# Optimization experiments

Hardware: AMD Instinct MI355X
Metric: run time of the kernel (lower is better)

The kernel has to match this reference:

```python
import jax, jax.numpy as jnp
import numpy as np

B, NF, N, D, S, H = 16, 16, 1024, 128, 8, 128
EPS = 1e-8
SCALE = D ** -0.5


def _ln(x, g, b):
    m = x.mean(-1, keepdims=True)
    v = ((x - m) ** 2).mean(-1, keepdims=True)
    return (x - m) / jnp.sqrt(v + 1e-5) * g + b


def setup_inputs() -> dict:
    key = jax.random.key(0)
    ks = jax.random.split(key, 16)
    w = lambda k, *s: jax.random.normal(k, s, jnp.float32) * 0.02
    return {
        'inputs': jax.random.normal(ks[0], (B, NF, N, D), jnp.float32),
        'slots_init': jax.random.normal(ks[1], (1, S, D), jnp.float32),
        'Wq': w(ks[2], D, D), 'bq': jnp.zeros((D,), jnp.float32),
        'Wk': w(ks[3], D, D), 'bk': jnp.zeros((D,), jnp.float32),
        'Wv': w(ks[4], D, D), 'bv': jnp.zeros((D,), jnp.float32),
        'W1': w(ks[5], H, D), 'b1': jnp.zeros((H,), jnp.float32),
        'W2': w(ks[6], D, H), 'b2': jnp.zeros((D,), jnp.float32),
        'Wih': w(ks[7], 3 * D, D), 'Whh': w(ks[8], 3 * D, D),
        'bih': jnp.zeros((3 * D,), jnp.float32), 'bhh': jnp.zeros((3 * D,), jnp.float32),
        'g_in': jnp.ones((D,), jnp.float32), 'be_in': jnp.zeros((D,), jnp.float32),
        'g_sl': jnp.ones((D,), jnp.float32), 'be_sl': jnp.zeros((D,), jnp.float32),
        'g_ff': jnp.ones((D,), jnp.float32), 'be_ff': jnp.zeros((D,), jnp.float32),
    }


def reference(inputs, slots_init, Wq, bq, Wk, bk, Wv, bv, W1, b1, W2, b2,
              Wih, Whh, bih, bhh, g_in, be_in, g_sl, be_sl, g_ff, be_ff):
    def gru(x, h):  # PyTorch GRUCell, x/h: [BS, D]
        gi = x @ Wih.T + bih
        gh = h @ Whh.T + bhh
        r = jax.nn.sigmoid(gi[:, :D] + gh[:, :D])
        z = jax.nn.sigmoid(gi[:, D:2 * D] + gh[:, D:2 * D])
        n = jnp.tanh(gi[:, 2 * D:] + r * gh[:, 2 * D:])
        return (1.0 - z) * n + z * h

    def get_attention(slots, x):  # slots [B,S,D], x [B,N,D]
        slots_prev = slots
        xn = _ln(x, g_in, be_in)
        k = xn @ Wk.T + bk
        v = xn @ Wv.T + bv
        q = _ln(slots, g_sl, be_sl) @ Wq.T + bq
        dots = jnp.einsum('bid,bjd->bij', q, k) * SCALE  # [B,S,N]
        attn_ori = jax.nn.softmax(dots, axis=1) + EPS    # softmax over slots
        attn = attn_ori / attn_ori.sum(axis=-1, keepdims=True)
        updates = jnp.einsum('bjd,bij->bid', v, attn)    # [B,S,D]
        slots = gru(updates.reshape(-1, D), slots_prev.reshape(-1, D)).reshape(slots.shape[0], -1, D)
        ff = jax.nn.relu(_ln(slots, g_ff, be_ff) @ W1.T + b1) @ W2.T + b2
        return slots + ff, attn_ori

    slots = jnp.broadcast_to(slots_init, (inputs.shape[0], S, D))
    slots, _ = get_attention(slots, inputs[:, 0])  # warm-up on frame 0

    def body(carry, x_f):
        s, a = get_attention(carry, x_f)
        return s, (s, a)

    _, (slots_seq, attn_seq) = jax.lax.scan(body, slots, jnp.moveaxis(inputs, 1, 0))
    slots_out = jnp.moveaxis(slots_seq, 0, 1)  # [B,NF,S,D]
    attns = jnp.moveaxis(attn_seq, 0, 1)       # [B,NF,S,N]
    return slots_out, attns
```

## Files before the change

kernel.cpp:

```cpp
#include <hip/hip_runtime.h>

#define B_ 16
#define NF_ 16
#define N_ 1024
#define D_ 128
#define S_ 8
#define SCALE_ 0.08838834764831845f
#define NB 256
#define NT 512

struct SmemA {
  float Xt[64 * 129];
  float qWs[1024];
  float at[512];
  float rowsum[64], rowsum2[64];
  float qbs[8];
};
struct SmemB {
  float Pk[128], upd[128], hn[128], buf[128], hid[128], qsh[128], nrm[128];
  float gi[384], gh[384];
  float red[4], ssm;
};
union Smem { SmemA a; SmemB b; };

__device__ __forceinline__ float gload(const float* p) {
  return __hip_atomic_load(p, __ATOMIC_RELAXED, __HIP_MEMORY_SCOPE_AGENT);
}
__device__ __forceinline__ void gstore(float* p, float v) {
  __hip_atomic_store(p, v, __ATOMIC_RELAXED, __HIP_MEMORY_SCOPE_AGENT);
}

__device__ __forceinline__ void arrive(unsigned* c) {
  __syncthreads();
  if (threadIdx.x == 0) {
    __builtin_amdgcn_s_waitcnt(0);
    __hip_atomic_fetch_add(c, 1u, __ATOMIC_RELAXED, __HIP_MEMORY_SCOPE_AGENT);
  }
}
__device__ __forceinline__ void wait_for(unsigned* c, unsigned target) {
  if (threadIdx.x == 0) {
    while (__hip_atomic_load(c, __ATOMIC_RELAXED, __HIP_MEMORY_SCOPE_AGENT) < target)
      __builtin_amdgcn_s_sleep(1);
  }
  __syncthreads();
}

__device__ __forceinline__ float dot128f(const float* __restrict__ wrow, const float* x, float acc) {
  const float4* w = (const float4*)wrow;
#pragma unroll
  for (int i = 0; i < 32; ++i) {
    float4 v = w[i];
    const float4 xv = *(const float4*)(x + i * 4);
    acc += v.x * xv.x + v.y * xv.y + v.z * xv.z + v.w * xv.w;
  }
  return acc;
}

__device__ __forceinline__ void stats128(float v, int t, float* red, float& m, float& inv, float eps) {
  __syncthreads();
  float s = (t < 128) ? v : 0.f;
  float s2 = (t < 128) ? v * v : 0.f;
#pragma unroll
  for (int off = 32; off; off >>= 1) { s += __shfl_down(s, off); s2 += __shfl_down(s2, off); }
  if (t == 0)  { red[0] = s; red[2] = s2; }
  if (t == 64) { red[1] = s; red[3] = s2; }
  __syncthreads();
  m = (red[0] + red[1]) * (1.f / 128.f);
  float var = (red[2] + red[3]) * (1.f / 128.f) - m * m;
  inv = rsqrtf(var + eps);
}

__device__ __forceinline__ float sigm(float x) { return 1.f / (1.f + __expf(-x)); }
__device__ __forceinline__ float tanh_f(float x) { return 1.f - 2.f / (1.f + __expf(2.f * x)); }

__device__ void q_project(SmemB& B, const float* slot,
    const float* __restrict__ g_sl, const float* __restrict__ be_sl,
    const float* __restrict__ Wq, const float* __restrict__ bq,
    const float* __restrict__ Wk, const float* __restrict__ bk,
    float* qW_g, float* qb_g, int bs) {
  int t = threadIdx.x;
  float m, inv;
  float sv = (t < 128) ? slot[t] : 0.f;
  stats128(sv, t, B.red, m, inv, 1e-5f);
  if (t < 128) B.nrm[t] = (sv - m) * inv * g_sl[t] + be_sl[t];
  __syncthreads();
  if (t < 128) B.qsh[t] = dot128f(Wq + t * 128, B.nrm, bq[t]);
  __syncthreads();
  if (t < 128) {
    float a = 0.f;
#pragma unroll 16
    for (int d = 0; d < 128; ++d) a += B.qsh[d] * Wk[d * 128 + t];
    gstore(&qW_g[bs * 128 + t], a);
    float p = B.qsh[t] * bk[t];
#pragma unroll
    for (int off = 32; off; off >>= 1) p += __shfl_down(p, off);
    if (t == 0)  B.red[0] = p;
    if (t == 64) B.red[1] = p;
  }
  __syncthreads();
  if (t == 0) gstore(&qb_g[bs], B.red[0] + B.red[1]);
}

__global__ __launch_bounds__(NT) void slot_persist(
    const float* __restrict__ x, const float* __restrict__ slots_init,
    const float* __restrict__ Wq, const float* __restrict__ bq,
    const float* __restrict__ Wk, const float* __restrict__ bk,
    const float* __restrict__ Wv, const float* __restrict__ bv,
    const float* __restrict__ W1, const float* __restrict__ b1,
    const float* __restrict__ W2, const float* __restrict__ b2,
    const float* __restrict__ Wih, const float* __restrict__ Whh,
    const float* __restrict__ bih, const float* __restrict__ bhh,
    const float* __restrict__ g_in, const float* __restrict__ be_in,
    const float* __restrict__ g_sl, const float* __restrict__ be_sl,
    const float* __restrict__ g_ff, const float* __restrict__ be_ff,
    float* out_slots, float* out_attn,
    unsigned* cntA, unsigned* cntB,
    float* qW_g, float* qb_g, float* P_part, float* S_part) {
  __shared__ __align__(16) Smem sm;
  __shared__ __align__(16) float slot_sh[128];
  __shared__ float gs[128], bs_[128];
  int t = threadIdx.x, bid = blockIdx.x;
  int b = bid >> 4, jt = bid & 15;
  bool isB = (jt < 8);
  unsigned* cA = cntA + (b << 6);
  unsigned* cB = cntB + (b << 6);

  if (t < 128) { gs[t] = g_in[t]; bs_[t] = be_in[t]; }
  if (isB) {
    if (t < 128) slot_sh[t] = slots_init[jt * 128 + t];
    q_project(sm.b, slot_sh, g_sl, be_sl, Wq, bq, Wk, bk, qW_g, qb_g, b * 8 + jt);
    arrive(cB);
  }
  float4 pf[4];
  {
    const float* xsrc = x + (((long)b * NF_ + 0) * N_ + jt * 64) * D_;
#pragma unroll
    for (int i = 0; i < 4; ++i) {
      int ch = t + i * 512;
      pf[i] = *(const float4*)(xsrc + (ch >> 5) * 128 + (ch & 31) * 4);
    }
  }
  wait_for(cB, 8u);

  for (int it = 0; it < 17; ++it) {
    int f = (it == 0) ? 0 : it - 1;
    int wo = it > 0;
#pragma unroll
    for (int i = 0; i < 4; ++i) {
      int ch = t + i * 512;
      float* dst = sm.a.Xt + (ch >> 5) * 129 + (ch & 31) * 4;
      dst[0] = pf[i].x; dst[1] = pf[i].y; dst[2] = pf[i].z; dst[3] = pf[i].w;
    }
    sm.a.qWs[t] = gload(&qW_g[b * 1024 + t]);
    sm.a.qWs[512 + t] = gload(&qW_g[b * 1024 + 512 + t]);
    if (t < 8) sm.a.qbs[t] = gload(&qb_g[b * 8 + t]);
    __syncthreads();
    int r8 = t >> 3, p8 = t & 7;
    {
      const float* row = sm.a.Xt + r8 * 129 + p8 * 16;
      float s1 = 0.f, s2 = 0.f;
#pragma unroll
      for (int i = 0; i < 16; ++i) { float v = row[i]; s1 += v; s2 += v * v; }
      s1 += __shfl_down(s1, 1); s2 += __shfl_down(s2, 1);
      s1 += __shfl_down(s1, 2); s2 += __shfl_down(s2, 2);
      s1 += __shfl_down(s1, 4); s2 += __shfl_down(s2, 4);
      if (p8 == 0) { sm.a.rowsum[r8] = s1; sm.a.rowsum2[r8] = s2; }
    }
    __syncthreads();
    {
      float m = sm.a.rowsum[r8] * (1.f / 128.f);
      float var = sm.a.rowsum2[r8] * (1.f / 128.f) - m * m;
      float inv = rsqrtf(var + 1e-5f);
      float* row = sm.a.Xt + r8 * 129 + p8 * 16;
      const float* gg = gs + p8 * 16;
      const float* bb = bs_ + p8 * 16;
#pragma unroll
      for (int i = 0; i < 16; ++i) row[i] = (row[i] - m) * inv * gg[i] + bb[i];
    }
    __syncthreads();
    {
      int s = t >> 6, j = t & 63;
      const float* qq = sm.a.qWs + s * 128;
      const float* xr = sm.a.Xt + j * 129;
      float d = 0.f;
#pragma unroll
      for (int k = 0; k < 128; ++k) d += xr[k] * qq[k];
      sm.a.at[s * 64 + j] = (d + sm.a.qbs[s]) * SCALE_;
    }
    __syncthreads();
    if (t < 64) {
      float vals[8], mx = -1e30f;
#pragma unroll
      for (int s = 0; s < 8; ++s) { vals[s] = sm.a.at[s * 64 + t]; mx = fmaxf(mx, vals[s]); }
      float sum = 0.f;
#pragma unroll
      for (int s = 0; s < 8; ++s) { vals[s] = __expf(vals[s] - mx); sum += vals[s]; }
      float rr = 1.f / sum;
#pragma unroll
      for (int s = 0; s < 8; ++s) { vals[s] = vals[s] * rr + 1e-8f; sm.a.at[s * 64 + t] = vals[s]; }
      if (wo) {
#pragma unroll
        for (int s = 0; s < 8; ++s)
          out_attn[(((long)b * NF_ + f) * S_ + s) * N_ + jt * 64 + t] = vals[s];
      }
    }
    __syncthreads();
    {
      int w = t >> 6, lane = t & 63;
      float v = sm.a.at[w * 64 + lane];
#pragma unroll
      for (int off = 32; off; off >>= 1) v += __shfl_down(v, off);
      if (lane == 0) gstore(&S_part[(b * 16 + jt) * 8 + w], v);
    }
    {
      int k2 = t & 127, h = t >> 7;
      float u0 = 0.f, u1 = 0.f;
      const float* a0 = sm.a.at + h * 64;
      const float* a1 = sm.a.at + (h + 4) * 64;
#pragma unroll 8
      for (int j = 0; j < 64; ++j) {
        float xv = sm.a.Xt[j * 129 + k2];
        u0 += xv * a0[j]; u1 += xv * a1[j];
      }
      float* pp = P_part + (long)(b * 16 + jt) * 8 * 128;
      gstore(&pp[h * 128 + k2], u0);
      gstore(&pp[(h + 4) * 128 + k2], u1);
    }
    arrive(cA);
    if (it < 16) {
      const float* xsrc = x + (((long)b * NF_ + it) * N_ + jt * 64) * D_;
#pragma unroll
      for (int i = 0; i < 4; ++i) {
        int ch = t + i * 512;
        pf[i] = *(const float4*)(xsrc + (ch >> 5) * 128 + (ch & 31) * 4);
      }
    }
    if (isB) {
      wait_for(cA, 16u * (it + 1));
      SmemB& B = sm.b;
      int s = jt;
      if (t < 128) {
        float pa = 0.f;
#pragma unroll
        for (int j = 0; j < 16; ++j)
          pa += gload(&P_part[(long)((b * 16 + j) * 8 + s) * 128 + t]);
        B.Pk[t] = pa;
      }
      if (t < 16) {
        float sv = gload(&S_part[(b * 16 + t) * 8 + s]);
        sv += __shfl_down(sv, 8); sv += __shfl_down(sv, 4);
        sv += __shfl_down(sv, 2); sv += __shfl_down(sv, 1);
        if (t == 0) B.ssm = sv;
      }
      __syncthreads();
      if (t < 128) {
        float a = dot128f(Wv + t * 128, B.Pk, 0.f);
        B.upd[t] = a / B.ssm + bv[t];
      } else {
        int r = t - 128;
        B.gh[r] = dot128f(Whh + r * 128, slot_sh, bhh[r]);
      }
      __syncthreads();
      if (t < 384) B.gi[t] = dot128f(Wih + t * 128, B.upd, bih[t]);
      __syncthreads();
      if (t < 128) {
        float r = sigm(B.gi[t] + B.gh[t]);
        float z = sigm(B.gi[128 + t] + B.gh[128 + t]);
        float n = tanh_f(B.gi[256 + t] + r * B.gh[256 + t]);
        B.hn[t] = (1.f - z) * n + z * slot_sh[t];
      }
      float m, inv;
      float hv = (t < 128) ? B.hn[t] : 0.f;
      stats128(hv, t, B.red, m, inv, 1e-5f);
      if (t < 128) B.buf[t] = (hv - m) * inv * g_ff[t] + be_ff[t];
      __syncthreads();
      if (t < 128) B.hid[t] = fmaxf(dot128f(W1 + t * 128, B.buf, b1[t]), 0.f);
      __syncthreads();
      if (t < 128) {
        float ffv = dot128f(W2 + t * 128, B.hid, b2[t]);
        float sn = B.hn[t] + ffv;
        slot_sh[t] = sn;
        if (wo) out_slots[(((long)b * NF_ + f) * S_ + s) * D_ + t] = sn;
      }
      __syncthreads();
      if (it < 16) {
        q_project(B, slot_sh, g_sl, be_sl, Wq, bq, Wk, bk, qW_g, qb_g, b * 8 + s);
        arrive(cB);
        wait_for(cB, 8u * (it + 2));
      }
    } else {
      if (it < 16) wait_for(cB, 8u * (it + 2));
    }
  }
}

extern "C" void kernel_launch(void* const* d_in, const int* in_sizes, int n_in,
                              void* d_out, int out_size, void* d_ws, size_t ws_size,
                              hipStream_t stream) {
  const float* inputs     = (const float*)d_in[0];
  const float* slots_init = (const float*)d_in[1];
  const float* Wq  = (const float*)d_in[2];
  const float* bq  = (const float*)d_in[3];
  const float* Wk  = (const float*)d_in[4];
  const float* bk  = (const float*)d_in[5];
  const float* Wv  = (const float*)d_in[6];
  const float* bv  = (const float*)d_in[7];
  const float* W1  = (const float*)d_in[8];
  const float* b1  = (const float*)d_in[9];
  const float* W2  = (const float*)d_in[10];
  const float* b2  = (const float*)d_in[11];
  const float* Wih = (const float*)d_in[12];
  const float* Whh = (const float*)d_in[13];
  const float* bih = (const float*)d_in[14];
  const float* bhh = (const float*)d_in[15];
  const float* g_in  = (const float*)d_in[16];
  const float* be_in = (const float*)d_in[17];
  const float* g_sl  = (const float*)d_in[18];
  const float* be_sl = (const float*)d_in[19];
  const float* g_ff  = (const float*)d_in[20];
  const float* be_ff = (const float*)d_in[21];

  float* out_slots = (float*)d_out;
  float* out_attn  = out_slots + (size_t)B_ * NF_ * S_ * D_;

  char* ws = (char*)d_ws;
  unsigned* cntA = (unsigned*)ws;
  unsigned* cntB = (unsigned*)(ws + 4096);
  float* qW_g    = (float*)(ws + 16384);
  float* qb_g    = (float*)(ws + 16384 + 65536);
  float* P_part  = (float*)(ws + 16384 + 66048);
  float* S_part  = (float*)(ws + 16384 + 66048 + 1048576);

  hipMemsetAsync(d_ws, 0, 16384, stream);

  slot_persist<<<NB, NT, 0, stream>>>(inputs, slots_init, Wq, bq, Wk, bk, Wv, bv,
      W1, b1, W2, b2, Wih, Whh, bih, bhh, g_in, be_in, g_sl, be_sl, g_ff, be_ff,
      out_slots, out_attn, cntA, cntB, qW_g, qb_g, P_part, S_part);
}
```

Before: 775.8 us.

## Fold LayerNorm and projections into precomputed weights, one grid barrier per frame

A precompute kernel now builds fused weight products once: Wih·Wv, the Wk-Wq product, and the matching bias terms. The input LayerNorm is folded algebraically into the attention logits and the update, so keys and values are never materialized. The persistent kernel is restructured to 128 blocks of 1024 threads, each handling 128 tokens and all 8 slots. Every block redundantly recomputes the GRU, the MLP and the next query, which removes the second cross-block barrier and the separate slot-update blocks. Partial sums are double-buffered by parity. The cost is duplicated slot work in each block and heavier shared-memory staging of weights.

```diff
diff --git a/kernel.cpp b/kernel.cpp
--- a/kernel.cpp
+++ b/kernel.cpp
@@ -5,23 +5,33 @@
 #define N_ 1024
 #define D_ 128
 #define S_ 8
+#define NT 1024
 #define SCALE_ 0.08838834764831845f
-#define NB 256
-#define NT 512
-
-struct SmemA {
-  float Xt[64 * 129];
-  float qWs[1024];
-  float at[512];
-  float rowsum[64], rowsum2[64];
-  float qbs[8];
+
+struct PA {
+  float X[128 * 129];
+  float at[8 * 132];
+  float ap[8 * 132];
+  float mean[128], rinv[128];
 };
-struct SmemB {
-  float Pk[128], upd[128], hn[128], buf[128], hid[128], qsh[128], nrm[128];
-  float gi[384], gh[384];
-  float red[4], ssm;
+struct PB {
+  float WL[128 * 132];
+  float part[4 * 8 * 128];
+  float Pn[8 * 132];
+  float gh[8 * 388];
+  float gi[8 * 388];
+  float hn[8 * 132];
+  float buf[8 * 132];
+  float hid[8 * 132];
 };
-union Smem { SmemA a; SmemB b; };
+union SMU { PA a; PB b; };
+struct Per {
+  float h[8 * 132];
+  float gqW[8 * 132];
+  float gI[128], bI[128], gF[128], bF[128], gS[128], bS[128];
+  float c0s[8], c1s[8], qbs[8], ssp[8], mbp[8], invSS[8];
+  float red[48];
+};
 
 __device__ __forceinline__ float gload(const float* p) {
   return __hip_atomic_load(p, __ATOMIC_RELAXED, __HIP_MEMORY_SCOPE_AGENT);
@@ -29,7 +39,6 @@
 __device__ __forceinline__ void gstore(float* p, float v) {
   __hip_atomic_store(p, v, __ATOMIC_RELAXED, __HIP_MEMORY_SCOPE_AGENT);
 }
-
 __device__ __forceinline__ void arrive(unsigned* c) {
   __syncthreads();
   if (threadIdx.x == 0) {
@@ -44,253 +53,360 @@
   }
   __syncthreads();
 }
-
-__device__ __forceinline__ float dot128f(const float* __restrict__ wrow, const float* x, float acc) {
-  const float4* w = (const float4*)wrow;
-#pragma unroll
-  for (int i = 0; i < 32; ++i) {
-    float4 v = w[i];
-    const float4 xv = *(const float4*)(x + i * 4);
-    acc += v.x * xv.x + v.y * xv.y + v.z * xv.z + v.w * xv.w;
-  }
-  return acc;
-}
-
-__device__ __forceinline__ void stats128(float v, int t, float* red, float& m, float& inv, float eps) {
-  __syncthreads();
-  float s = (t < 128) ? v : 0.f;
-  float s2 = (t < 128) ? v * v : 0.f;
-#pragma unroll
-  for (int off = 32; off; off >>= 1) { s += __shfl_down(s, off); s2 += __shfl_down(s2, off); }
-  if (t == 0)  { red[0] = s; red[2] = s2; }
-  if (t == 64) { red[1] = s; red[3] = s2; }
-  __syncthreads();
-  m = (red[0] + red[1]) * (1.f / 128.f);
-  float var = (red[2] + red[3]) * (1.f / 128.f) - m * m;
-  inv = rsqrtf(var + eps);
-}
-
 __device__ __forceinline__ float sigm(float x) { return 1.f / (1.f + __expf(-x)); }
 __device__ __forceinline__ float tanh_f(float x) { return 1.f - 2.f / (1.f + __expf(2.f * x)); }
 
-__device__ void q_project(SmemB& B, const float* slot,
-    const float* __restrict__ g_sl, const float* __restrict__ be_sl,
+__device__ __forceinline__ void stage_w(float* WL, const float* __restrict__ W, int t) {
+#pragma unroll
+  for (int i = 0; i < 4; ++i) {
+    int idx = t + i * 1024;
+    int r = idx >> 5, k4 = idx & 31;
+    const float4 v = *(const float4*)(W + r * 128 + k4 * 4);
+    *(float4*)&WL[r * 132 + ((k4 ^ (r & 7)) << 2)] = v;
+  }
+}
+
+__device__ __forceinline__ void wmat8(SMU& sm, const float* vecs, int t) {
+  if (t < 512) {
+    int r = t & 127, kc = t >> 7;
+    float acc[8] = {0.f,0.f,0.f,0.f,0.f,0.f,0.f,0.f};
+#pragma unroll
+    for (int g = 0; g < 8; ++g) {
+      int k4 = kc * 8 + g;
+      const float4 wv = *(const float4*)&sm.b.WL[r * 132 + ((k4 ^ (r & 7)) << 2)];
+#pragma unroll
+      for (int s2 = 0; s2 < 8; ++s2) {
+        const float4 vv = *(const float4*)&vecs[s2 * 132 + k4 * 4];
+        acc[s2] += wv.x * vv.x + wv.y * vv.y + wv.z * vv.z + wv.w * vv.w;
+      }
+    }
+#pragma unroll
+    for (int s2 = 0; s2 < 8; ++s2) sm.b.part[(kc * 8 + s2) * 128 + r] = acc[s2];
+  }
+}
+
+__device__ void slot_to_qw(SMU& sm, Per& P,
+    const float* __restrict__ Wqk, const float* __restrict__ bqk,
+    const float* __restrict__ wqbk, const float* __restrict__ bqbk, int t) {
+  int s = t >> 7, d = t & 127, w = t >> 6, lane = t & 63;
+  float v = P.h[s * 132 + d];
+  float a1 = v, a2 = v * v;
+#pragma unroll
+  for (int off = 32; off; off >>= 1) { a1 += __shfl_down(a1, off); a2 += __shfl_down(a2, off); }
+  if (lane == 0) { P.red[w] = a1; P.red[16 + w] = a2; }
+  __syncthreads();
+  float m = (P.red[2 * s] + P.red[2 * s + 1]) * (1.f / 128.f);
+  float var = (P.red[16 + 2 * s] + P.red[16 + 2 * s + 1]) * (1.f / 128.f) - m * m;
+  float inv = rsqrtf(var + 1e-5f);
+  float nv = (v - m) * inv * P.gS[d] + P.bS[d];
+  sm.b.buf[s * 132 + d] = nv;
+  float qp = wqbk[d] * nv;
+#pragma unroll
+  for (int off = 32; off; off >>= 1) qp += __shfl_down(qp, off);
+  if (lane == 0) P.red[32 + w] = qp;
+  stage_w(sm.b.WL, Wqk, t);
+  __syncthreads();
+  if (t < 8) P.qbs[t] = P.red[32 + 2 * t] + P.red[32 + 2 * t + 1] + bqbk[0];
+  wmat8(sm, sm.b.buf, t);
+  __syncthreads();
+  {
+    int r = d;
+    float qv = bqk[r];
+#pragma unroll
+    for (int kc = 0; kc < 4; ++kc) qv += sm.b.part[(kc * 8 + s) * 128 + r];
+    float gq = P.gI[r] * qv;
+    P.gqW[s * 132 + r] = gq;
+    float p1 = gq, p0 = P.bI[r] * qv;
+#pragma unroll
+    for (int off = 32; off; off >>= 1) { p1 += __shfl_down(p1, off); p0 += __shfl_down(p0, off); }
+    if (lane == 0) { P.red[w] = p1; P.red[16 + w] = p0; }
+  }
+  __syncthreads();
+  if (t < 8) {
+    P.c1s[t] = P.red[2 * t] + P.red[2 * t + 1];
+    P.c0s[t] = P.red[16 + 2 * t] + P.red[16 + 2 * t + 1] + P.qbs[t];
+  }
+  __syncthreads();
+}
+
+__global__ __launch_bounds__(128) void precomp(
+    const float* __restrict__ Wih, const float* __restrict__ bih,
+    const float* __restrict__ Wv, const float* __restrict__ bv,
     const float* __restrict__ Wq, const float* __restrict__ bq,
     const float* __restrict__ Wk, const float* __restrict__ bk,
-    float* qW_g, float* qb_g, int bs) {
-  int t = threadIdx.x;
-  float m, inv;
-  float sv = (t < 128) ? slot[t] : 0.f;
-  stats128(sv, t, B.red, m, inv, 1e-5f);
-  if (t < 128) B.nrm[t] = (sv - m) * inv * g_sl[t] + be_sl[t];
-  __syncthreads();
-  if (t < 128) B.qsh[t] = dot128f(Wq + t * 128, B.nrm, bq[t]);
-  __syncthreads();
-  if (t < 128) {
-    float a = 0.f;
-#pragma unroll 16
-    for (int d = 0; d < 128; ++d) a += B.qsh[d] * Wk[d * 128 + t];
-    gstore(&qW_g[bs * 128 + t], a);
-    float p = B.qsh[t] * bk[t];
+    float* Wiv, float* bihv, float* Wqk, float* bqk, float* wqbk, float* bqbk) {
+  __shared__ float r2[2];
+  int r = blockIdx.x, t = threadIdx.x;
+  if (r < 384) {
+    float acc = 0.f;
+#pragma unroll 8
+    for (int k = 0; k < 128; ++k) acc += Wih[r * 128 + k] * Wv[k * 128 + t];
+    Wiv[r * 128 + t] = acc;
+    float p = Wih[r * 128 + t] * bv[t];
 #pragma unroll
     for (int off = 32; off; off >>= 1) p += __shfl_down(p, off);
-    if (t == 0)  B.red[0] = p;
-    if (t == 64) B.red[1] = p;
-  }
-  __syncthreads();
-  if (t == 0) gstore(&qb_g[bs], B.red[0] + B.red[1]);
-}
-
-__global__ __launch_bounds__(NT) void slot_persist(
+    if ((t & 63) == 0) r2[t >> 6] = p;
+    __syncthreads();
+    if (t == 0) bihv[r] = r2[0] + r2[1] + bih[r];
+  } else {
+    int c = r - 384;
+    float acc = 0.f;
+#pragma unroll 8
+    for (int dd = 0; dd < 128; ++dd) acc += Wk[dd * 128 + c] * Wq[dd * 128 + t];
+    Wqk[c * 128 + t] = acc;
+    float p = Wk[t * 128 + c] * bq[t];
+#pragma unroll
+    for (int off = 32; off; off >>= 1) p += __shfl_down(p, off);
+    if ((t & 63) == 0) r2[t >> 6] = p;
+    __syncthreads();
+    if (t == 0) bqk[c] = r2[0] + r2[1];
+    if (c == 0) {
+      float a2 = 0.f;
+#pragma unroll 8
+      for (int dd = 0; dd < 128; ++dd) a2 += Wq[dd * 128 + t] * bk[dd];
+      wqbk[t] = a2;
+      float p2 = bq[t] * bk[t];
+#pragma unroll
+      for (int off = 32; off; off >>= 1) p2 += __shfl_down(p2, off);
+      __syncthreads();
+      if ((t & 63) == 0) r2[t >> 6] = p2;
+      __syncthreads();
+      if (t == 0) bqbk[0] = r2[0] + r2[1];
+    }
+  }
+}
+
+__global__ __launch_bounds__(NT) void slot_fused(
     const float* __restrict__ x, const float* __restrict__ slots_init,
-    const float* __restrict__ Wq, const float* __restrict__ bq,
-    const float* __restrict__ Wk, const float* __restrict__ bk,
-    const float* __restrict__ Wv, const float* __restrict__ bv,
+    const float* __restrict__ Whh, const float* __restrict__ bhh,
     const float* __restrict__ W1, const float* __restrict__ b1,
     const float* __restrict__ W2, const float* __restrict__ b2,
-    const float* __restrict__ Wih, const float* __restrict__ Whh,
-    const float* __restrict__ bih, const float* __restrict__ bhh,
     const float* __restrict__ g_in, const float* __restrict__ be_in,
     const float* __restrict__ g_sl, const float* __restrict__ be_sl,
     const float* __restrict__ g_ff, const float* __restrict__ be_ff,
+    const float* __restrict__ Wiv, const float* __restrict__ bihv,
+    const float* __restrict__ Wqk, const float* __restrict__ bqk,
+    const float* __restrict__ wqbk, const float* __restrict__ bqbk,
     float* out_slots, float* out_attn,
-    unsigned* cntA, unsigned* cntB,
-    float* qW_g, float* qb_g, float* P_part, float* S_part) {
-  __shared__ __align__(16) Smem sm;
-  __shared__ __align__(16) float slot_sh[128];
-  __shared__ float gs[128], bs_[128];
+    unsigned* cnt, float* Ppart, float* Spart) {
+  __shared__ __align__(16) SMU sm;
+  __shared__ __align__(16) Per P;
   int t = threadIdx.x, bid = blockIdx.x;
-  int b = bid >> 4, jt = bid & 15;
-  bool isB = (jt < 8);
-  unsigned* cA = cntA + (b << 6);
-  unsigned* cB = cntB + (b << 6);
-
-  if (t < 128) { gs[t] = g_in[t]; bs_[t] = be_in[t]; }
-  if (isB) {
-    if (t < 128) slot_sh[t] = slots_init[jt * 128 + t];
-    q_project(sm.b, slot_sh, g_sl, be_sl, Wq, bq, Wk, bk, qW_g, qb_g, b * 8 + jt);
-    arrive(cB);
-  }
+  int b = bid >> 3, jb = bid & 7;
+  unsigned* cb = cnt + (b << 6);
+  int s = t >> 7, d = t & 127, w = t >> 6, lane = t & 63;
+
+  if (t < 128) {
+    P.gI[t] = g_in[t]; P.bI[t] = be_in[t];
+    P.gF[t] = g_ff[t]; P.bF[t] = be_ff[t];
+    P.gS[t] = g_sl[t]; P.bS[t] = be_sl[t];
+  }
+  P.h[s * 132 + d] = slots_init[s * 128 + d];
   float4 pf[4];
   {
-    const float* xsrc = x + (((long)b * NF_ + 0) * N_ + jt * 64) * D_;
+    const float* xs = x + ((long)b * NF_ * N_ + jb * 128) * D_;
 #pragma unroll
     for (int i = 0; i < 4; ++i) {
-      int ch = t + i * 512;
-      pf[i] = *(const float4*)(xsrc + (ch >> 5) * 128 + (ch & 31) * 4);
-    }
-  }
-  wait_for(cB, 8u);
-
-  for (int it = 0; it < 17; ++it) {
+      int ch = t + i * 1024;
+      pf[i] = *(const float4*)(xs + (ch >> 5) * 128 + (ch & 31) * 4);
+    }
+  }
+  __syncthreads();
+  slot_to_qw(sm, P, Wqk, bqk, wqbk, bqbk, t);
+
+  for (int it = 0; it <= 16; ++it) {
     int f = (it == 0) ? 0 : it - 1;
     int wo = it > 0;
+    int par = it & 1;
 #pragma unroll
     for (int i = 0; i < 4; ++i) {
-      int ch = t + i * 512;
-      float* dst = sm.a.Xt + (ch >> 5) * 129 + (ch & 31) * 4;
+      int ch = t + i * 1024;
+      float* dst = sm.a.X + (ch >> 5) * 129 + (ch & 31) * 4;
       dst[0] = pf[i].x; dst[1] = pf[i].y; dst[2] = pf[i].z; dst[3] = pf[i].w;
     }
-    sm.a.qWs[t] = gload(&qW_g[b * 1024 + t]);
-    sm.a.qWs[512 + t] = gload(&qW_g[b * 1024 + 512 + t]);
-    if (t < 8) sm.a.qbs[t] = gload(&qb_g[b * 8 + t]);
-    __syncthreads();
-    int r8 = t >> 3, p8 = t & 7;
-    {
-      const float* row = sm.a.Xt + r8 * 129 + p8 * 16;
+    __syncthreads();
+    {
+      int r = t >> 3, p8 = t & 7;
+      const float* row = sm.a.X + r * 129 + p8 * 16;
       float s1 = 0.f, s2 = 0.f;
 #pragma unroll
-      for (int i = 0; i < 16; ++i) { float v = row[i]; s1 += v; s2 += v * v; }
+      for (int i = 0; i < 16; ++i) { float vv = row[i]; s1 += vv; s2 += vv * vv; }
       s1 += __shfl_down(s1, 1); s2 += __shfl_down(s2, 1);
       s1 += __shfl_down(s1, 2); s2 += __shfl_down(s2, 2);
       s1 += __shfl_down(s1, 4); s2 += __shfl_down(s2, 4);
-      if (p8 == 0) { sm.a.rowsum[r8] = s1; sm.a.rowsum2[r8] = s2; }
-    }
-    __syncthreads();
-    {
-      float m = sm.a.rowsum[r8] * (1.f / 128.f);
-      float var = sm.a.rowsum2[r8] * (1.f / 128.f) - m * m;
+      if (p8 == 0) {
+        float m = s1 * (1.f / 128.f);
+        sm.a.mean[r] = m;
+        sm.a.rinv[r] = rsqrtf(s2 * (1.f / 128.f) - m * m + 1e-5f);
+      }
+    }
+    __syncthreads();
+    {
+      int j = d;
+      const float* xr = sm.a.X + j * 129;
+      const float* qr = P.gqW + s * 132;
+      float acc = 0.f;
+#pragma unroll 8
+      for (int k4 = 0; k4 < 32; ++k4) {
+        const float4 q4 = *(const float4*)&qr[k4 * 4];
+        acc += xr[k4 * 4 + 0] * q4.x + xr[k4 * 4 + 1] * q4.y +
+               xr[k4 * 4 + 2] * q4.z + xr[k4 * 4 + 3] * q4.w;
+      }
+      float val = (acc - sm.a.mean[j] * P.c1s[s]) * sm.a.rinv[j] + P.c0s[s];
+      sm.a.at[s * 132 + j] = val * SCALE_;
+    }
+    __syncthreads();
+    {
+      int j = d;
+      float vv[8]; float mx = -1e30f;
+#pragma unroll
+      for (int ss = 0; ss < 8; ++ss) { vv[ss] = sm.a.at[ss * 132 + j]; mx = fmaxf(mx, vv[ss]); }
+      float sum = 0.f, mine = 0.f;
+#pragma unroll
+      for (int ss = 0; ss < 8; ++ss) { float e = __expf(vv[ss] - mx); sum += e; if (ss == s) mine = e; }
+      float attn = mine / sum + 1e-8f;
+      if (wo) out_attn[(((long)b * NF_ + f) * S_ + s) * N_ + jb * 128 + j] = attn;
+      float riv = sm.a.rinv[j];
+      sm.a.ap[s * 132 + j] = attn * riv;
+      float a1 = attn, a2 = attn * sm.a.mean[j] * riv;
+#pragma unroll
+      for (int off = 32; off; off >>= 1) { a1 += __shfl_down(a1, off); a2 += __shfl_down(a2, off); }
+      if (lane == 0) { P.red[w] = a1; P.red[16 + w] = a2; }
+    }
+    __syncthreads();
+    if (t < 8) {
+      float* Spub = Spart + (((b * 2 + par) * 8 + jb) * 16);
+      gstore(&Spub[t], P.red[2 * t] + P.red[2 * t + 1]);
+      gstore(&Spub[8 + t], P.red[16 + 2 * t] + P.red[16 + 2 * t + 1]);
+    }
+    {
+      int k = t >> 3, jc = t & 7;
+      float acc[8] = {0.f,0.f,0.f,0.f,0.f,0.f,0.f,0.f};
+#pragma unroll
+      for (int j4 = 0; j4 < 4; ++j4) {
+        int j0 = jc * 16 + j4 * 4;
+        float xv0 = sm.a.X[(j0 + 0) * 129 + k];
+        float xv1 = sm.a.X[(j0 + 1) * 129 + k];
+        float xv2 = sm.a.X[(j0 + 2) * 129 + k];
+        float xv3 = sm.a.X[(j0 + 3) * 129 + k];
+#pragma unroll
+        for (int s2 = 0; s2 < 8; ++s2) {
+          const float4 av = *(const float4*)&sm.a.ap[s2 * 132 + j0];
+          acc[s2] += av.x * xv0 + av.y * xv1 + av.z * xv2 + av.w * xv3;
+        }
+      }
+#pragma unroll
+      for (int off = 1; off < 8; off <<= 1) {
+#pragma unroll
+        for (int s2 = 0; s2 < 8; ++s2) acc[s2] += __shfl_down(acc[s2], off);
+      }
+      if (jc == 0) {
+        float* Ppub = Ppart + (((b * 2 + par) * 8 + jb) * 1024);
+#pragma unroll
+        for (int s2 = 0; s2 < 8; ++s2) gstore(&Ppub[s2 * 128 + k], acc[s2]);
+      }
+    }
+    arrive(cb);
+    if (it < 16) {
+      const float* xs = x + (((long)b * NF_ + it) * N_ + jb * 128) * D_;
+#pragma unroll
+      for (int i = 0; i < 4; ++i) {
+        int ch = t + i * 1024;
+        pf[i] = *(const float4*)(xs + (ch >> 5) * 128 + (ch & 31) * 4);
+      }
+    }
+    wait_for(cb, 8u * (it + 1));
+    float uval = 0.f;
+    {
+      const float* Pp = Ppart + ((b * 2 + par) * 8) * 1024;
+#pragma unroll
+      for (int blk = 0; blk < 8; ++blk) uval += gload(&Pp[blk * 1024 + s * 128 + d]);
+    }
+    if (t < 64) {
+      int s2 = t >> 3, blk = t & 7;
+      const float* Sp = Spart + ((b * 2 + par) * 8) * 16;
+      float sv = gload(&Sp[blk * 16 + s2]);
+      float mv = gload(&Sp[blk * 16 + 8 + s2]);
+#pragma unroll
+      for (int off = 4; off; off >>= 1) { sv += __shfl_down(sv, off); mv += __shfl_down(mv, off); }
+      if (blk == 0) { P.ssp[s2] = sv; P.mbp[s2] = mv; P.invSS[s2] = 1.f / sv; }
+    }
+    __syncthreads();
+    sm.b.Pn[s * 132 + d] = P.gI[d] * (uval - P.mbp[s]) * P.invSS[s] + P.bI[d];
+    __syncthreads();
+    if (t < 384) {
+      int r0 = t * 2;
+      bool isH = t < 192;
+      const float* Wr = isH ? (Whh + (long)r0 * 128) : (Wiv + (long)(r0 - 384) * 128);
+      const float* vec = isH ? P.h : sm.b.Pn;
+      float bb0 = isH ? bhh[r0] : bihv[r0 - 384];
+      float bb1 = isH ? bhh[r0 + 1] : bihv[r0 - 383];
+      float a0[8] = {0.f,0.f,0.f,0.f,0.f,0.f,0.f,0.f};
+      float a1v[8] = {0.f,0.f,0.f,0.f,0.f,0.f,0.f,0.f};
+#pragma unroll 4
+      for (int k4 = 0; k4 < 32; ++k4) {
+        const float4 w0 = *(const float4*)(Wr + k4 * 4);
+        const float4 w1 = *(const float4*)(Wr + 128 + k4 * 4);
+#pragma unroll
+        for (int s2 = 0; s2 < 8; ++s2) {
+          const float4 vv = *(const float4*)&vec[s2 * 132 + k4 * 4];
+          a0[s2] += w0.x * vv.x + w0.y * vv.y + w0.z * vv.z + w0.w * vv.w;
+          a1v[s2] += w1.x * vv.x + w1.y * vv.y + w1.z * vv.z + w1.w * vv.w;
+        }
+      }
+      float* og = isH ? sm.b.gh : sm.b.gi;
+      int rr = isH ? r0 : r0 - 384;
+#pragma unroll
+      for (int s2 = 0; s2 < 8; ++s2) {
+        og[s2 * 388 + rr] = a0[s2] + bb0;
+        og[s2 * 388 + rr + 1] = a1v[s2] + bb1;
+      }
+    }
+    __syncthreads();
+    float hnew;
+    {
+      const float* gis = sm.b.gi + s * 388;
+      const float* ghs = sm.b.gh + s * 388;
+      float gr = sigm(gis[d] + ghs[d]);
+      float gz = sigm(gis[128 + d] + ghs[128 + d]);
+      float gn = tanh_f(gis[256 + d] + gr * ghs[256 + d]);
+      hnew = (1.f - gz) * gn + gz * P.h[s * 132 + d];
+      sm.b.hn[s * 132 + d] = hnew;
+      float a1 = hnew, a2 = hnew * hnew;
+#pragma unroll
+      for (int off = 32; off; off >>= 1) { a1 += __shfl_down(a1, off); a2 += __shfl_down(a2, off); }
+      if (lane == 0) { P.red[w] = a1; P.red[16 + w] = a2; }
+    }
+    __syncthreads();
+    {
+      float m = (P.red[2 * s] + P.red[2 * s + 1]) * (1.f / 128.f);
+      float var = (P.red[16 + 2 * s] + P.red[16 + 2 * s + 1]) * (1.f / 128.f) - m * m;
       float inv = rsqrtf(var + 1e-5f);
-      float* row = sm.a.Xt + r8 * 129 + p8 * 16;
-      const float* gg = gs + p8 * 16;
-      const float* bb = bs_ + p8 * 16;
-#pragma unroll
-      for (int i = 0; i < 16; ++i) row[i] = (row[i] - m) * inv * gg[i] + bb[i];
-    }
-    __syncthreads();
-    {
-      int s = t >> 6, j = t & 63;
-      const float* qq = sm.a.qWs + s * 128;
-      const float* xr = sm.a.Xt + j * 129;
-      float d = 0.f;
-#pragma unroll
-      for (int k = 0; k < 128; ++k) d += xr[k] * qq[k];
-      sm.a.at[s * 64 + j] = (d + sm.a.qbs[s]) * SCALE_;
-    }
-    __syncthreads();
-    if (t < 64) {
-      float vals[8], mx = -1e30f;
-#pragma unroll
-      for (int s = 0; s < 8; ++s) { vals[s] = sm.a.at[s * 64 + t]; mx = fmaxf(mx, vals[s]); }
-      float sum = 0.f;
-#pragma unroll
-      for (int s = 0; s < 8; ++s) { vals[s] = __expf(vals[s] - mx); sum += vals[s]; }
-      float rr = 1.f / sum;
-#pragma unroll
-      for (int s = 0; s < 8; ++s) { vals[s] = vals[s] * rr + 1e-8f; sm.a.at[s * 64 + t] = vals[s]; }
-      if (wo) {
-#pragma unroll
-        for (int s = 0; s < 8; ++s)
-          out_attn[(((long)b * NF_ + f) * S_ + s) * N_ + jt * 64 + t] = vals[s];
-      }
-    }
-    __syncthreads();
-    {
-      int w = t >> 6, lane = t & 63;
-      float v = sm.a.at[w * 64 + lane];
-#pragma unroll
-      for (int off = 32; off; off >>= 1) v += __shfl_down(v, off);
-      if (lane == 0) gstore(&S_part[(b * 16 + jt) * 8 + w], v);
-    }
-    {
-      int k2 = t & 127, h = t >> 7;
-      float u0 = 0.f, u1 = 0.f;
-      const float* a0 = sm.a.at + h * 64;
-      const float* a1 = sm.a.at + (h + 4) * 64;
-#pragma unroll 8
-      for (int j = 0; j < 64; ++j) {
-        float xv = sm.a.Xt[j * 129 + k2];
-        u0 += xv * a0[j]; u1 += xv * a1[j];
-      }
-      float* pp = P_part + (long)(b * 16 + jt) * 8 * 128;
-      gstore(&pp[h * 128 + k2], u0);
-      gstore(&pp[(h + 4) * 128 + k2], u1);
-    }
-    arrive(cA);
-    if (it < 16) {
-      const float* xsrc = x + (((long)b * NF_ + it) * N_ + jt * 64) * D_;
-#pragma unroll
-      for (int i = 0; i < 4; ++i) {
-        int ch = t + i * 512;
-        pf[i] = *(const float4*)(xsrc + (ch >> 5) * 128 + (ch & 31) * 4);
-      }
-    }
-    if (isB) {
-      wait_for(cA, 16u * (it + 1));
-      SmemB& B = sm.b;
-      int s = jt;
-      if (t < 128) {
-        float pa = 0.f;
-#pragma unroll
-        for (int j = 0; j < 16; ++j)
-          pa += gload(&P_part[(long)((b * 16 + j) * 8 + s) * 128 + t]);
-        B.Pk[t] = pa;
-      }
-      if (t < 16) {
-        float sv = gload(&S_part[(b * 16 + t) * 8 + s]);
-        sv += __shfl_down(sv, 8); sv += __shfl_down(sv, 4);
-        sv += __shfl_down(sv, 2); sv += __shfl_down(sv, 1);
-        if (t == 0) B.ssm = sv;
-      }
-      __syncthreads();
-      if (t < 128) {
-        float a = dot128f(Wv + t * 128, B.Pk, 0.f);
-        B.upd[t] = a / B.ssm + bv[t];
-      } else {
-        int r = t - 128;
-        B.gh[r] = dot128f(Whh + r * 128, slot_sh, bhh[r]);
-      }
-      __syncthreads();
-      if (t < 384) B.gi[t] = dot128f(Wih + t * 128, B.upd, bih[t]);
-      __syncthreads();
-      if (t < 128) {
-        float r = sigm(B.gi[t] + B.gh[t]);
-        float z = sigm(B.gi[128 + t] + B.gh[128 + t]);
-        float n = tanh_f(B.gi[256 + t] + r * B.gh[256 + t]);
-        B.hn[t] = (1.f - z) * n + z * slot_sh[t];
-      }
-      float m, inv;
-      float hv = (t < 128) ? B.hn[t] : 0.f;
-      stats128(hv, t, B.red, m, inv, 1e-5f);
-      if (t < 128) B.buf[t] = (hv - m) * inv * g_ff[t] + be_ff[t];
-      __syncthreads();
-      if (t < 128) B.hid[t] = fmaxf(dot128f(W1 + t * 128, B.buf, b1[t]), 0.f);
-      __syncthreads();
-      if (t < 128) {
-        float ffv = dot128f(W2 + t * 128, B.hid, b2[t]);
-        float sn = B.hn[t] + ffv;
-        slot_sh[t] = sn;
-        if (wo) out_slots[(((long)b * NF_ + f) * S_ + s) * D_ + t] = sn;
-      }
-      __syncthreads();
-      if (it < 16) {
-        q_project(B, slot_sh, g_sl, be_sl, Wq, bq, Wk, bk, qW_g, qb_g, b * 8 + s);
-        arrive(cB);
-        wait_for(cB, 8u * (it + 2));
-      }
-    } else {
-      if (it < 16) wait_for(cB, 8u * (it + 2));
-    }
+      sm.b.buf[s * 132 + d] = (hnew - m) * inv * P.gF[d] + P.bF[d];
+    }
+    stage_w(sm.b.WL, W1, t);
+    __syncthreads();
+    wmat8(sm, sm.b.buf, t);
+    __syncthreads();
+    {
+      float hv = b1[d];
+#pragma unroll
+      for (int kc = 0; kc < 4; ++kc) hv += sm.b.part[(kc * 8 + s) * 128 + d];
+      sm.b.hid[s * 132 + d] = fmaxf(hv, 0.f);
+    }
+    stage_w(sm.b.WL, W2, t);
+    __syncthreads();
+    wmat8(sm, sm.b.hid, t);
+    __syncthreads();
+    {
+      float ff = b2[d];
+#pragma unroll
+      for (int kc = 0; kc < 4; ++kc) ff += sm.b.part[(kc * 8 + s) * 128 + d];
+      float sn = sm.b.hn[s * 132 + d] + ff;
+      P.h[s * 132 + d] = sn;
+      if (wo) out_slots[(((long)b * NF_ + f) * S_ + s) * D_ + d] = sn;
+    }
+    if (it < 16) slot_to_qw(sm, P, Wqk, bqk, wqbk, bqbk, t);
   }
 }
 
@@ -324,16 +440,21 @@
   float* out_attn  = out_slots + (size_t)B_ * NF_ * S_ * D_;
 
   char* ws = (char*)d_ws;
-  unsigned* cntA = (unsigned*)ws;
-  unsigned* cntB = (unsigned*)(ws + 4096);
-  float* qW_g    = (float*)(ws + 16384);
-  float* qb_g    = (float*)(ws + 16384 + 65536);
-  float* P_part  = (float*)(ws + 16384 + 66048);
-  float* S_part  = (float*)(ws + 16384 + 66048 + 1048576);
-
-  hipMemsetAsync(d_ws, 0, 16384, stream);
-
-  slot_persist<<<NB, NT, 0, stream>>>(inputs, slots_init, Wq, bq, Wk, bk, Wv, bv,
-      W1, b1, W2, b2, Wih, Whh, bih, bhh, g_in, be_in, g_sl, be_sl, g_ff, be_ff,
-      out_slots, out_attn, cntA, cntB, qW_g, qb_g, P_part, S_part);
-}
+  unsigned* cnt = (unsigned*)ws;
+  float* Wiv   = (float*)(ws + 4096);
+  float* bihv  = (float*)(ws + 201728 - 1024);
+  float* Wqk   = (float*)(ws + 202240);
+  float* bqk   = (float*)(ws + 267776);
+  float* wqbk  = (float*)(ws + 268288);
+  float* bqbk  = (float*)(ws + 268800);
+  float* Ppart = (float*)(ws + 269056);
+  float* Spart = (float*)(ws + 269056 + 1048576);
+
+  hipMemsetAsync(d_ws, 0, 4096, stream);
+
+  precomp<<<512, 128, 0, stream>>>(Wih, bih, Wv, bv, Wq, bq, Wk, bk,
+                                   Wiv, bihv, Wqk, bqk, wqbk, bqbk);
+  slot_fused<<<128, NT, 0, stream>>>(inputs, slots_init, Whh, bhh, W1, b1, W2, b2,
+      g_in, be_in, g_sl, be_sl, g_ff, be_ff, Wiv, bihv, Wqk, bqk, wqbk, bqbk,
+      out_slots, out_attn, cnt, Ppart, Spart);
+}
```

New measurement: 1.032 ms. 1.33x slower.
